# Kernel tuning notes

Measured on AMD Instinct MI355X. Metric: run time of the kernel, lower is better.

Reference implementation:

```python
import jax, jax.numpy as jnp
import numpy as np

NS = 50000; ND = 50000; E = 600000
C = 64; A = 16; S = 64; H = 8; M = 192; DH = C // H
EPS = 1e-5


def _ln(x, w, b):
    # EquivariantLayerNormV2 restricted to 0e irreps == standard affine LayerNorm
    x = x - jnp.mean(x, axis=-1, keepdims=True)
    v = jnp.mean(x * x, axis=-1, keepdims=True)
    return x * jax.lax.rsqrt(v + EPS) * w + b


def _forward(src_f, dst_f, edge_attr, edge_scalars, edge_logits, edge_src, edge_dst,
             ln_src_w, ln_src_b, W_src, ln_dst_w, ln_dst_b, W_dst, b_dst,
             W_ea, W_dtp, W_r1, b_r1, W_r2, b_r2, alpha_vec,
             W_proj, b_proj, ln_post_w, ln_post_b, W_f1, b_f1, W_f2, b_f2):
    # prenorm + linear projections of src/dst node features
    ms = _ln(src_f, ln_src_w, ln_src_b) @ W_src                      # [NS, C]
    md = _ln(dst_f, ln_dst_w, ln_dst_b) @ W_dst + b_dst              # [ND, C]
    msg = ms[edge_src] + md[edge_dst]                                # [E, C] gather
    # radial MLP on edge scalars modulates the (scalar-irrep) tensor-product weights
    r = jax.nn.silu(edge_scalars @ W_r1 + b_r1)                      # [E, S]
    w_edge = r @ W_r2 + b_r2                                         # [E, 2C]
    ea = edge_attr @ W_ea                                            # [E, C]
    dtp = ((msg * ea) @ W_dtp) * w_edge                              # [E, 2C]
    alpha_feat = dtp[:, :C].reshape(E, H, DH)
    val = dtp[:, C:].reshape(E, H, DH)
    # per-head attention logits + optional precomputed edge logits
    logits = jnp.sum(jax.nn.leaky_relu(alpha_feat, 0.2) * alpha_vec, axis=-1)  # [E, H]
    logits = logits + edge_logits[:, None]
    # softmax over incoming edges of each dst node (segment softmax)
    m = jax.ops.segment_max(logits, edge_dst, num_segments=ND)
    a = jnp.exp(logits - m[edge_dst])
    z = jax.ops.segment_sum(a, edge_dst, num_segments=ND)
    attn = a / z[edge_dst]                                           # [E, H]
    out = jax.ops.segment_sum((val * attn[..., None]).reshape(E, C), edge_dst,
                              num_segments=ND)                       # [ND, C] scatter
    out = out @ W_proj + b_proj
    emb = out + dst_f                                                # skip_1 (irreps match -> identity)
    y = _ln(emb, ln_post_w, ln_post_b)                               # post_norm
    ffn = jax.nn.silu(y @ W_f1 + b_f1) @ W_f2 + b_f2                 # FFN with swish gate (0e)
    return ffn + emb                                                 # skip_2


def setup_inputs() -> dict:
    key = jax.random.key(0)
    ks = jax.random.split(key, 20)
    def n(k, shape, scale=1.0):
        return jax.random.normal(k, shape, dtype=jnp.float32) * scale
    return {
        "src_f": n(ks[0], (NS, C)),
        "dst_f": n(ks[1], (ND, C)),
        "edge_attr": n(ks[2], (E, A)),
        "edge_scalars": jax.random.uniform(ks[3], (E, S), dtype=jnp.float32),
        "edge_logits": n(ks[4], (E,)),
        "edge_src": jax.random.randint(ks[5], (E,), 0, NS),
        "edge_dst": jax.random.randint(ks[6], (E,), 0, ND),
        "ln_src_w": jnp.ones((C,), jnp.float32), "ln_src_b": jnp.zeros((C,), jnp.float32),
        "W_src": n(ks[7], (C, C), C ** -0.5),
        "ln_dst_w": jnp.ones((C,), jnp.float32), "ln_dst_b": jnp.zeros((C,), jnp.float32),
        "W_dst": n(ks[8], (C, C), C ** -0.5), "b_dst": jnp.zeros((C,), jnp.float32),
        "W_ea": n(ks[9], (A, C), A ** -0.5),
        "W_dtp": n(ks[10], (C, 2 * C), C ** -0.5),
        "W_r1": n(ks[11], (S, S), S ** -0.5), "b_r1": jnp.zeros((S,), jnp.float32),
        "W_r2": n(ks[12], (S, 2 * C), S ** -0.5), "b_r2": jnp.zeros((2 * C,), jnp.float32),
        "alpha_vec": n(ks[13], (H, DH), DH ** -0.5),
        "W_proj": n(ks[14], (C, C), C ** -0.5), "b_proj": jnp.zeros((C,), jnp.float32),
        "ln_post_w": jnp.ones((C,), jnp.float32), "ln_post_b": jnp.zeros((C,), jnp.float32),
        "W_f1": n(ks[15], (C, M), C ** -0.5), "b_f1": jnp.zeros((M,), jnp.float32),
        "W_f2": n(ks[16], (M, C), M ** -0.5), "b_f2": jnp.zeros((C,), jnp.float32),
    }


def reference(src_f, dst_f, edge_attr, edge_scalars, edge_logits, edge_src, edge_dst,
              ln_src_w, ln_src_b, W_src, ln_dst_w, ln_dst_b, W_dst, b_dst,
              W_ea, W_dtp, W_r1, b_r1, W_r2, b_r2, alpha_vec,
              W_proj, b_proj, ln_post_w, ln_post_b, W_f1, b_f1, W_f2, b_f2):
    return _forward(src_f, dst_f, edge_attr, edge_scalars, edge_logits, edge_src, edge_dst,
                    ln_src_w, ln_src_b, W_src, ln_dst_w, ln_dst_b, W_dst, b_dst,
                    W_ea, W_dtp, W_r1, b_r1, W_r2, b_r2, alpha_vec,
                    W_proj, b_proj, ln_post_w, ln_post_b, W_f1, b_f1, W_f2, b_f2)
```

## Files before the change

kernel.cpp:

```cpp
#include <hip/hip_runtime.h>
#include <hip/hip_bf16.h>

typedef __hip_bfloat16 bf16;
typedef unsigned short u16;
typedef unsigned int u32;

#define NS_N 50000
#define ND_N 50000
#define NE_E 600000
#define C 64
#define AD 16
#define SD 64
#define NH 8
#define MF 192
#define EPSV 1e-5f

#define WB() __builtin_amdgcn_wave_barrier()

typedef short short8 __attribute__((ext_vector_type(8)));
typedef float f32x4 __attribute__((ext_vector_type(4)));
#define MFMA16(a, b, c) __builtin_amdgcn_mfma_f32_16x16x32_bf16(a, b, c, 0, 0, 0)

__device__ __forceinline__ float lo16(u32 u) {
    union { u32 i; float f; } v; v.i = u << 16; return v.f;
}
__device__ __forceinline__ float hi16(u32 u) {
    union { u32 i; float f; } v; v.i = u & 0xffff0000u; return v.f;
}
__device__ __forceinline__ float b2fu(u16 u) {
    union { u32 i; float f; } v; v.i = ((u32)u) << 16; return v.f;
}
__device__ __forceinline__ u16 f2bbits(float f) {
    u32 u = __float_as_uint(f);
    u32 r = u + 0x7FFFu + ((u >> 16) & 1u);
    return (u16)(r >> 16);
}
__device__ __forceinline__ float loadf(const void* p, size_t i, int isbf) {
    if (isbf) { union { u32 u; float f; } v; v.u = ((u32)((const u16*)p)[i]) << 16; return v.f; }
    return ((const float*)p)[i];
}
__device__ __forceinline__ u16 loadb(const void* p, size_t i, int isbf) {
    if (isbf) return ((const u16*)p)[i];
    return f2bbits(((const float*)p)[i]);
}
__device__ __forceinline__ short8 load8bf(const void* p, size_t off, int isbf) {
    if (isbf) return *(const short8*)((const u16*)p + off);
    const float4* q = (const float4*)((const float*)p + off);
    float4 f0 = q[0], f1 = q[1];
    short8 r;
    r[0] = (short)f2bbits(f0.x); r[1] = (short)f2bbits(f0.y);
    r[2] = (short)f2bbits(f0.z); r[3] = (short)f2bbits(f0.w);
    r[4] = (short)f2bbits(f1.x); r[5] = (short)f2bbits(f1.y);
    r[6] = (short)f2bbits(f1.z); r[7] = (short)f2bbits(f1.w);
    return r;
}

__device__ __forceinline__ float waveAllSum(float v) {
    #pragma unroll
    for (int off = 32; off >= 1; off >>= 1) v += __shfl_xor(v, off, 64);
    return v;
}

__global__ void detect_zero_kernel(const void* src, int* flag, int* cnt) {
    if (blockIdx.x == 0) {
        if (threadIdx.x < 64) {
            const u16* p = (const u16*)src;
            const int lane = threadIdx.x;
            int c = 0;
            #pragma unroll
            for (int j = 0; j < 32; ++j) {
                u16 w = p[(size_t)(lane * 32 + j) * 2];
                int e = (w >> 7) & 0xFF;
                if (w == 0 || (e >= 100 && e <= 150)) c++;
            }
            #pragma unroll
            for (int off = 32; off >= 1; off >>= 1) c += __shfl_xor(c, off, 64);
            if (lane == 0) *flag = (c > 1536) ? 1 : 0;
        }
    } else {
        int i = (blockIdx.x - 1) * blockDim.x + threadIdx.x;
        if (i < ND_N) cnt[i] = 0;
    }
}

__global__ void hist_kernel(const int* __restrict__ edge_dst, int* __restrict__ cnt) {
    int e = blockIdx.x * blockDim.x + threadIdx.x;
    if (e < NE_E) atomicAdd(&cnt[edge_dst[e]], 1);
}

#define SCAN_CHUNK 1024
#define SCAN_NCH ((ND_N + SCAN_CHUNK - 1) / SCAN_CHUNK)

__global__ void scan_phase1(const int* __restrict__ cnt, int* __restrict__ chunksum) {
    __shared__ int wsum[4];
    const int b = blockIdx.x, tidx = threadIdx.x;
    const int base = b * SCAN_CHUNK + tidx * 4;
    int s = 0;
    if (base + 3 < ND_N) {
        int4 v = *(const int4*)&cnt[base];
        s = v.x + v.y + v.z + v.w;
    } else {
        #pragma unroll
        for (int j = 0; j < 4; ++j) { int i = base + j; if (i < ND_N) s += cnt[i]; }
    }
    #pragma unroll
    for (int off = 32; off >= 1; off >>= 1) s += __shfl_xor(s, off, 64);
    const int wv = tidx >> 6, lane = tidx & 63;
    if (lane == 0) wsum[wv] = s;
    __syncthreads();
    if (tidx == 0) chunksum[b] = wsum[0] + wsum[1] + wsum[2] + wsum[3];
}

__global__ void scan_phase3(const int* __restrict__ cnt, const int* __restrict__ chunksum,
                            int* __restrict__ row_ptr, int* __restrict__ cursor,
                            int* __restrict__ row_ptr_last) {
    __shared__ int woff[4];
    __shared__ int choff_s;
    const int b = blockIdx.x, tidx = threadIdx.x;
    if (tidx < 64) {
        int v = (tidx < SCAN_NCH) ? chunksum[tidx] : 0;
        int incl = v;
        #pragma unroll
        for (int off = 1; off < 64; off <<= 1) {
            int t = __shfl_up(incl, off, 64);
            if (tidx >= off) incl += t;
        }
        if (tidx == b) choff_s = incl - v;
        if (b == 0 && tidx == 63) *row_ptr_last = incl;
    }
    const int base = b * SCAN_CHUNK + tidx * 4;
    int v[4];
    #pragma unroll
    for (int j = 0; j < 4; ++j) { int i = base + j; v[j] = (i < ND_N) ? cnt[i] : 0; }
    int s = v[0] + v[1] + v[2] + v[3];
    int incl = s;
    const int lane = tidx & 63, wv = tidx >> 6;
    #pragma unroll
    for (int off = 1; off < 64; off <<= 1) {
        int t = __shfl_up(incl, off, 64);
        if (lane >= off) incl += t;
    }
    if (lane == 63) woff[wv] = incl;
    __syncthreads();
    int cross = 0;
    for (int w = 0; w < wv; ++w) cross += woff[w];
    int run = choff_s + cross + (incl - s);
    #pragma unroll
    for (int j = 0; j < 4; ++j) {
        int i = base + j;
        if (i < ND_N) { row_ptr[i] = run; cursor[i] = run; }
        run += v[j];
    }
}

__global__ void scatter_kernel(const int* __restrict__ edge_dst, int* __restrict__ cursor,
                               int* __restrict__ perm) {
    int e = blockIdx.x * blockDim.x + threadIdx.x;
    if (e < NE_E) {
        int pos = atomicAdd(&cursor[edge_dst[e]], 1);
        perm[pos] = e;
    }
}

__launch_bounds__(512)
__global__ void node_proj2_mfma(const void* __restrict__ src_f, const void* __restrict__ dst_f,
                                const void* __restrict__ lnw_s, const void* __restrict__ lnb_s,
                                const void* __restrict__ W_s,
                                const void* __restrict__ lnw_d, const void* __restrict__ lnb_d,
                                const void* __restrict__ W_d, const void* __restrict__ b_d,
                                const int* __restrict__ flagp,
                                u16* __restrict__ ms, u16* __restrict__ md) {
    __shared__ u16 sWT[2][C * C];
    __shared__ float slnw2[2][C], slnb2[2][C], sbias[C];
    __shared__ u16 scratch[8][16 * C];

    const int isbf = *flagp;
    const int tid = threadIdx.x;
    for (int i = tid; i < C * C; i += 512) {
        int k = i >> 6, n = i & 63;
        int off = n * 64 + (((k >> 3) ^ (n & 7)) << 3) + (k & 7);
        sWT[0][off] = loadb(W_s, i, isbf);
        sWT[1][off] = loadb(W_d, i, isbf);
    }
    for (int i = tid; i < C; i += 512) {
        slnw2[0][i] = loadf(lnw_s, i, isbf);
        slnb2[0][i] = loadf(lnb_s, i, isbf);
        slnw2[1][i] = loadf(lnw_d, i, isbf);
        slnb2[1][i] = loadf(lnb_d, i, isbf);
        sbias[i] = loadf(b_d, i, isbf);
    }
    __syncthreads();

    const int wv = tid >> 6, lane = tid & 63;
    const int m15 = lane & 15, quad = lane >> 4;
    const int sw = m15 & 7;
    const int pg0 = (quad ^ sw) << 3;
    const int pg1 = pg0 ^ 32;
    u16* scr = scratch[wv];

    const int HT = NS_N / 16;
    const int NTILE = 2 * HT;
    for (int t = blockIdx.x * 8 + wv; t < NTILE; t += gridDim.x * 8) {
        const int half = (t >= HT) ? 1 : 0;
        const int n0 = (half ? (t - HT) : t) * 16;
        const void* xf = half ? dst_f : src_f;
        u16* out = half ? md : ms;
        float x0[8], x1[8];
        {
            size_t base = (size_t)(n0 + m15) * C + quad * 8;
            if (isbf) {
                short8 aa = *(const short8*)((const u16*)xf + base);
                short8 bb = *(const short8*)((const u16*)xf + base + 32);
                #pragma unroll
                for (int j = 0; j < 8; ++j) {
                    x0[j] = b2fu((u16)aa[j]);
                    x1[j] = b2fu((u16)bb[j]);
                }
            } else {
                const float* xp = (const float*)xf + base;
                float4 a0 = *(const float4*)xp;
                float4 a1 = *(const float4*)(xp + 4);
                float4 b0 = *(const float4*)(xp + 32);
                float4 b1 = *(const float4*)(xp + 36);
                x0[0] = a0.x; x0[1] = a0.y; x0[2] = a0.z; x0[3] = a0.w;
                x0[4] = a1.x; x0[5] = a1.y; x0[6] = a1.z; x0[7] = a1.w;
                x1[0] = b0.x; x1[1] = b0.y; x1[2] = b0.z; x1[3] = b0.w;
                x1[4] = b1.x; x1[5] = b1.y; x1[6] = b1.z; x1[7] = b1.w;
            }
        }
        float s = 0.f;
        #pragma unroll
        for (int j = 0; j < 8; ++j) s += x0[j] + x1[j];
        s += __shfl_xor(s, 16, 64);
        s += __shfl_xor(s, 32, 64);
        float mean = s * (1.f / 64.f);
        float q = 0.f;
        #pragma unroll
        for (int j = 0; j < 8; ++j) {
            float d0 = x0[j] - mean, d1 = x1[j] - mean;
            q += d0 * d0 + d1 * d1;
        }
        q += __shfl_xor(q, 16, 64);
        q += __shfl_xor(q, 32, 64);
        float rs = rsqrtf(q * (1.f / 64.f) + EPSV);
        short8 xA0, xA1;
        #pragma unroll
        for (int j = 0; j < 8; ++j) {
            int c0 = quad * 8 + j, c1 = 32 + quad * 8 + j;
            xA0[j] = (short)f2bbits((x0[j] - mean) * rs * slnw2[half][c0] + slnb2[half][c0]);
            xA1[j] = (short)f2bbits((x1[j] - mean) * rs * slnw2[half][c1] + slnb2[half][c1]);
        }
        WB();
        const u16* wT = sWT[half];
        #pragma unroll
        for (int nt = 0; nt < 4; ++nt) {
            f32x4 c = {0.f, 0.f, 0.f, 0.f};
            c = MFMA16(xA0, *(const short8*)&wT[(nt * 16 + m15) * 64 + pg0], c);
            c = MFMA16(xA1, *(const short8*)&wT[(nt * 16 + m15) * 64 + pg1], c);
            float bb = half ? sbias[nt * 16 + m15] : 0.f;
            int lg = nt * 2 + (m15 >> 3);
            int o = m15 & 7;
            #pragma unroll
            for (int r = 0; r < 4; ++r) {
                float v = c[r] + bb;
                int row = quad * 4 + r;
                scr[row * 64 + ((lg ^ (row & 7)) << 3) + o] = f2bbits(v);
            }
        }
        WB();
        {
            int row = lane >> 2, seg = lane & 3;
            int rw7 = row & 7;
            uint4 v0 = *(const uint4*)&scr[row * 64 + (((seg * 2) ^ rw7) << 3)];
            uint4 v1 = *(const uint4*)&scr[row * 64 + (((seg * 2 + 1) ^ rw7) << 3)];
            uint4* gp = (uint4*)&out[(size_t)(n0 + row) * C + seg * 16];
            gp[0] = v0; gp[1] = v1;
        }
        WB();
    }
}

__launch_bounds__(512, 4)
__global__ void edge_mfma_kernel(const void* __restrict__ edge_attr,
                                 const void* __restrict__ edge_scalars,
                                 const void* __restrict__ edge_logits,
                                 const int* __restrict__ edge_src,
                                 const int* __restrict__ edge_dst,
                                 const int* __restrict__ perm,
                                 const void* __restrict__ W_ea, const void* __restrict__ W_dtp,
                                 const void* __restrict__ W_r1, const void* __restrict__ b_r1,
                                 const void* __restrict__ W_r2, const void* __restrict__ b_r2,
                                 const void* __restrict__ alpha_vec,
                                 const int* __restrict__ flagp,
                                 const u16* __restrict__ ms, const u16* __restrict__ md,
                                 u16* __restrict__ valbuf, float* __restrict__ logitsbuf) {
    __shared__ u16 sWr1T[C * SD];
    __shared__ u16 sWr2T[2 * C * SD];
    __shared__ u16 sWdtpT[2 * C * C];
    __shared__ u16 sWeaT[C * 32];
    __shared__ float sbr1[SD], sbr2[2 * C], salpha[C];
    __shared__ u16 scratch[8][2][16 * C];

    const int isbf = *flagp;
    const int tid = threadIdx.x;
    for (int i = tid; i < SD * SD; i += 512) {
        int k = i >> 6, n = i & 63;
        sWr1T[n * 64 + (((k >> 3) ^ (n & 7)) << 3) + (k & 7)] = loadb(W_r1, i, isbf);
    }
    for (int i = tid; i < SD * 2 * C; i += 512) {
        int k = i >> 7, n = i & 127;
        sWr2T[n * 64 + (((k >> 3) ^ (n & 7)) << 3) + (k & 7)] = loadb(W_r2, i, isbf);
    }
    for (int i = tid; i < C * 2 * C; i += 512) {
        int k = i >> 7, n = i & 127;
        sWdtpT[n * 64 + (((k >> 3) ^ (n & 7)) << 3) + (k & 7)] = loadb(W_dtp, i, isbf);
    }
    for (int i = tid; i < C * 32; i += 512) {
        int n = i >> 5, k = i & 31;
        sWeaT[i] = (k < AD) ? loadb(W_ea, (size_t)k * C + n, isbf) : (u16)0;
    }
    for (int i = tid; i < SD; i += 512) sbr1[i] = loadf(b_r1, i, isbf);
    for (int i = tid; i < 2 * C; i += 512) sbr2[i] = loadf(b_r2, i, isbf);
    for (int i = tid; i < C; i += 512) salpha[i] = loadf(alpha_vec, i, isbf);
    __syncthreads();

    const int wv = tid >> 6, lane = tid & 63;
    const int m15 = lane & 15, quad = lane >> 4;
    const int sw = m15 & 7;
    const int pg0 = (quad ^ sw) << 3;
    const int pg1 = pg0 ^ 32;
    u16* scr_r = scratch[wv][0];
    u16* scr_e = scratch[wv][1];

    const int NT = NE_E / 16;
    const int stride = gridDim.x * 8;
    int t = blockIdx.x * 8 + wv;

    int e = 0, s = 0, dd = 0;
    if (t < NT) {
        e = perm[t * 16 + m15];
        s = edge_src[e];
        dd = edge_dst[e];
    }

    while (t < NT) {
        const int tn = t + stride;
        const int e0 = t * 16;
        short8 esA0 = load8bf(edge_scalars, (size_t)e * SD + quad * 8, isbf);
        short8 esA1 = load8bf(edge_scalars, (size_t)e * SD + 32 + quad * 8, isbf);
        float elg_lane = loadf(edge_logits, e, isbf);
        short8 eaA = 0;
        if (quad < 2) eaA = load8bf(edge_attr, (size_t)e * AD + quad * 8, isbf);
        const u16* msr = ms + (size_t)s * C;
        const u16* mdr = md + (size_t)dd * C;
        short8 gms0 = *(const short8*)&msr[quad * 8];
        short8 gms1 = *(const short8*)&msr[32 + quad * 8];
        short8 gmd0 = *(const short8*)&mdr[quad * 8];
        short8 gmd1 = *(const short8*)&mdr[32 + quad * 8];
        int eN = 0;
        if (tn < NT) eN = perm[tn * 16 + m15];
        WB();
        #pragma unroll
        for (int nt = 0; nt < 4; ++nt) {
            f32x4 c = {0.f, 0.f, 0.f, 0.f};
            c = MFMA16(esA0, *(const short8*)&sWr1T[(nt * 16 + m15) * 64 + pg0], c);
            c = MFMA16(esA1, *(const short8*)&sWr1T[(nt * 16 + m15) * 64 + pg1], c);
            float bc = sbr1[nt * 16 + m15];
            int lg = nt * 2 + (m15 >> 3);
            int o = m15 & 7;
            #pragma unroll
            for (int r = 0; r < 4; ++r) {
                float f = c[r] + bc;
                f = f / (1.f + __expf(-f));
                int row = quad * 4 + r;
                scr_r[row * 64 + ((lg ^ (row & 7)) << 3) + o] = f2bbits(f);
            }
        }
        #pragma unroll
        for (int nt = 0; nt < 4; ++nt) {
            f32x4 c = {0.f, 0.f, 0.f, 0.f};
            c = MFMA16(eaA, *(const short8*)&sWeaT[(nt * 16 + m15) * 32 + quad * 8], c);
            int lg = nt * 2 + (m15 >> 3);
            int o = m15 & 7;
            #pragma unroll
            for (int r = 0; r < 4; ++r) {
                int row = quad * 4 + r;
                scr_e[row * 64 + ((lg ^ (row & 7)) << 3) + o] = f2bbits(c[r]);
            }
        }
        int sN = 0, ddN = 0;
        if (tn < NT) { sN = edge_src[eN]; ddN = edge_dst[eN]; }
        WB();
        short8 rA0 = *(const short8*)&scr_r[m15 * 64 + pg0];
        short8 rA1 = *(const short8*)&scr_r[m15 * 64 + pg1];
        short8 ev0 = *(const short8*)&scr_e[m15 * 64 + pg0];
        short8 ev1 = *(const short8*)&scr_e[m15 * 64 + pg1];
        short8 xA0, xA1;
        #pragma unroll
        for (int j = 0; j < 8; ++j) {
            float a = b2fu((u16)gms0[j]) + b2fu((u16)gmd0[j]);
            xA0[j] = (short)f2bbits(a * b2fu((u16)ev0[j]));
            float b = b2fu((u16)gms1[j]) + b2fu((u16)gmd1[j]);
            xA1[j] = (short)f2bbits(b * b2fu((u16)ev1[j]));
        }
        float elg_q[4];
        #pragma unroll
        for (int r = 0; r < 4; ++r) elg_q[r] = __shfl(elg_lane, quad * 4 + r, 64);
        WB();
        #pragma unroll
        for (int nt = 0; nt < 8; ++nt) {
            f32x4 w = {0.f, 0.f, 0.f, 0.f};
            w = MFMA16(rA0, *(const short8*)&sWr2T[(nt * 16 + m15) * 64 + pg0], w);
            w = MFMA16(rA1, *(const short8*)&sWr2T[(nt * 16 + m15) * 64 + pg1], w);
            f32x4 dv = {0.f, 0.f, 0.f, 0.f};
            dv = MFMA16(xA0, *(const short8*)&sWdtpT[(nt * 16 + m15) * 64 + pg0], dv);
            dv = MFMA16(xA1, *(const short8*)&sWdtpT[(nt * 16 + m15) * 64 + pg1], dv);
            float wb = sbr2[nt * 16 + m15];
            if (nt < 4) {
                float sa = salpha[nt * 16 + m15];
                #pragma unroll
                for (int r = 0; r < 4; ++r) {
                    float v = dv[r] * (w[r] + wb);
                    float lf = (v >= 0.f) ? v : 0.2f * v;
                    float tt = lf * sa;
                    tt += __shfl_xor(tt, 1, 64);
                    tt += __shfl_xor(tt, 2, 64);
                    tt += __shfl_xor(tt, 4, 64);
                    if ((lane & 7) == 0)
                        logitsbuf[(size_t)(e0 + quad * 4 + r) * NH + nt * 2 + ((lane >> 3) & 1)]
                            = tt + elg_q[r];
                }
            } else {
                int lg = (nt - 4) * 2 + (m15 >> 3);
                int o = m15 & 7;
                #pragma unroll
                for (int r = 0; r < 4; ++r) {
                    float v = dv[r] * (w[r] + wb);
                    int row = quad * 4 + r;
                    scr_r[row * 64 + ((lg ^ (row & 7)) << 3) + o] = f2bbits(v);
                }
            }
        }
        WB();
        {
            int row = lane >> 2, seg = lane & 3;
            int rw7 = row & 7;
            uint4 v0 = *(const uint4*)&scr_r[row * 64 + (((seg * 2) ^ rw7) << 3)];
            uint4 v1 = *(const uint4*)&scr_r[row * 64 + (((seg * 2 + 1) ^ rw7) << 3)];
            uint4* gp = (uint4*)&valbuf[(size_t)(e0 + row) * C + seg * 16];
            gp[0] = v0; gp[1] = v1;
        }
        WB();
        t = tn; e = eN; s = sN; dd = ddN;
    }
}

__global__ void aggregate_kernel(const int* __restrict__ row_ptr,
                                 const float* __restrict__ logitsbuf,
                                 const u16* __restrict__ valbuf,
                                 float* __restrict__ attout) {
    const int wave = threadIdx.x >> 6, lane = threadIdx.x & 63;
    const int h = lane & 31;
    const int parity = lane >> 5;
    const int head = h >> 2;
    const int gw = blockIdx.x * 4 + wave, nw = gridDim.x * 4;
    const float NINF = -1e30f;
    for (int d = gw; d < ND_N; d += nw) {
        const int beg = row_ptr[d], end = row_ptr[d + 1];
        float m0 = NINF, z0 = 0.f, a00 = 0.f, a01 = 0.f;
        float m1 = NINF, z1 = 0.f, a10 = 0.f, a11 = 0.f;
        for (int i = beg + parity; i < end; i += 4) {
            u32 pv = *(const u32*)&valbuf[(size_t)i * C + 2 * h];
            float lg = logitsbuf[(size_t)i * NH + head];
            float mn = fmaxf(m0, lg);
            float sc = __expf(m0 - mn);
            float e = __expf(lg - mn);
            z0 = z0 * sc + e;
            a00 = a00 * sc + e * lo16(pv);
            a01 = a01 * sc + e * hi16(pv);
            m0 = mn;
        }
        for (int i = beg + parity + 2; i < end; i += 4) {
            u32 pv = *(const u32*)&valbuf[(size_t)i * C + 2 * h];
            float lg = logitsbuf[(size_t)i * NH + head];
            float mn = fmaxf(m1, lg);
            float sc = __expf(m1 - mn);
            float e = __expf(lg - mn);
            z1 = z1 * sc + e;
            a10 = a10 * sc + e * lo16(pv);
            a11 = a11 * sc + e * hi16(pv);
            m1 = mn;
        }
        float ma = fmaxf(m0, m1);
        float s0 = __expf(m0 - ma), s1 = __expf(m1 - ma);
        float z = z0 * s0 + z1 * s1;
        float a0 = a00 * s0 + a10 * s1;
        float a1 = a01 * s0 + a11 * s1;
        float mo = __shfl_xor(ma, 32, 64);
        float zo = __shfl_xor(z, 32, 64);
        float b0 = __shfl_xor(a0, 32, 64);
        float b1 = __shfl_xor(a1, 32, 64);
        float mm = fmaxf(ma, mo);
        float se = __expf(ma - mm), so = __expf(mo - mm);
        z = z * se + zo * so;
        a0 = a0 * se + b0 * so;
        a1 = a1 * se + b1 * so;
        if (parity == 0) {
            float2 r;
            r.x = (z > 0.f) ? a0 / z : 0.f;
            r.y = (z > 0.f) ? a1 / z : 0.f;
            *(float2*)&attout[(size_t)d * C + 2 * h] = r;
        }
    }
}

__global__ void edge_csr_kernel(const void* __restrict__ edge_attr,
                                const void* __restrict__ edge_scalars,
                                const void* __restrict__ edge_logits,
                                const int* __restrict__ edge_src,
                                const int* __restrict__ row_ptr, const int* __restrict__ perm,
                                const void* __restrict__ W_ea, const void* __restrict__ W_dtp,
                                const void* __restrict__ W_r1, const void* __restrict__ b_r1,
                                const void* __restrict__ W_r2, const void* __restrict__ b_r2,
                                const void* __restrict__ alpha_vec,
                                const int* __restrict__ flagp,
                                const u16* __restrict__ ms, const u16* __restrict__ md,
                                float* __restrict__ attout) {
    __shared__ u16 sWr1[SD * SD];
    __shared__ u16 sWr2[SD * 2 * C];
    __shared__ u16 sWdtp[C * 2 * C];
    __shared__ u16 sWea[AD * C];
    __shared__ float sbr1[SD], sbr2[2 * C], salpha[C];
    __shared__ float sbuf[4][2][C];

    const int isbf = *flagp;
    const int tid = threadIdx.x;
    {
        for (int i = tid; i < SD * SD; i += blockDim.x) {
            int k = i >> 6, c = i & 63;
            sWr1[((k >> 1) << 7) + (c << 1) + (k & 1)] = loadb(W_r1, i, isbf);
        }
        for (int i = tid; i < SD * 2 * C; i += blockDim.x) {
            int k = i >> 7, c = i & 127;
            sWr2[(k << 7) + ((c & 63) << 1) + (c >> 6)] = loadb(W_r2, i, isbf);
        }
        for (int i = tid; i < C * 2 * C; i += blockDim.x) {
            int k = i >> 7, c = i & 127;
            sWdtp[(k << 7) + ((c & 63) << 1) + (c >> 6)] = loadb(W_dtp, i, isbf);
        }
        for (int i = tid; i < AD * C; i += blockDim.x) {
            int k = i >> 6, c = i & 63;
            sWea[((k >> 1) << 7) + (c << 1) + (k & 1)] = loadb(W_ea, i, isbf);
        }
        for (int i = tid; i < SD; i += blockDim.x) sbr1[i] = loadf(b_r1, i, isbf);
        for (int i = tid; i < 2 * C; i += blockDim.x) sbr2[i] = loadf(b_r2, i, isbf);
        for (int i = tid; i < C; i += blockDim.x) salpha[i] = loadf(alpha_vec, i, isbf);
    }
    __syncthreads();

    const int wave = tid >> 6, lane = tid & 63;
    float* buf0 = sbuf[wave][0];
    float* buf1 = sbuf[wave][1];
    const u32* wr1 = (const u32*)sWr1;
    const u32* wr2 = (const u32*)sWr2;
    const u32* wdtp = (const u32*)sWdtp;
    const u32* wea = (const u32*)sWea;
    const int gw = blockIdx.x * 4 + wave, nw = gridDim.x * 4;

    for (int d = gw; d < ND_N; d += nw) {
        const int beg = row_ptr[d], end = row_ptr[d + 1];
        const float mdv = b2fu(md[(size_t)d * C + lane]);
        float m = -__builtin_inff(), z = 0.f, acc = 0.f;

        for (int i = beg; i < end; ++i) {
            const int e = perm[i];
            WB();
            buf0[lane] = loadf(edge_scalars, (size_t)e * SD + lane, isbf);
            WB();
            float accr = sbr1[lane];
            #pragma unroll 8
            for (int k2 = 0; k2 < 32; ++k2) {
                float2 xv = *(const float2*)&buf0[k2 * 2];
                u32 wp = wr1[(k2 << 6) + lane];
                accr += xv.x * lo16(wp) + xv.y * hi16(wp);
            }
            float r = accr / (1.f + __expf(-accr));
            WB();
            buf1[lane] = r;
            WB();
            float we0 = sbr2[lane], we1 = sbr2[lane + C];
            #pragma unroll 8
            for (int k = 0; k < SD; ++k) {
                float rk = buf1[k];
                u32 wp = wr2[(k << 6) + lane];
                we0 += rk * lo16(wp);
                we1 += rk * hi16(wp);
            }
            WB();
            if (lane < AD) buf0[lane] = loadf(edge_attr, (size_t)e * AD + lane, isbf);
            WB();
            float eav = 0.f;
            #pragma unroll
            for (int k2 = 0; k2 < 8; ++k2) {
                float2 xv = *(const float2*)&buf0[k2 * 2];
                u32 wp = wea[(k2 << 6) + lane];
                eav += xv.x * lo16(wp) + xv.y * hi16(wp);
            }
            const int s = edge_src[e];
            float x = (b2fu(ms[(size_t)s * C + lane]) + mdv) * eav;
            WB();
            buf1[lane] = x;
            WB();
            float dt0 = 0.f, dt1 = 0.f;
            #pragma unroll 8
            for (int k = 0; k < C; ++k) {
                float xk = buf1[k];
                u32 wp = wdtp[(k << 6) + lane];
                dt0 += xk * lo16(wp);
                dt1 += xk * hi16(wp);
            }
            dt0 *= we0;
            dt1 *= we1;
            float lf = (dt0 >= 0.f) ? dt0 : 0.2f * dt0;
            float t = lf * salpha[lane];
            t += __shfl_xor(t, 1, 64);
            t += __shfl_xor(t, 2, 64);
            t += __shfl_xor(t, 4, 64);
            float lg = t + loadf(edge_logits, e, isbf);
            float mn = fmaxf(m, lg);
            float sc = __expf(m - mn);
            float a = __expf(lg - mn);
            z = z * sc + a;
            acc = acc * sc + a * dt1;
            m = mn;
        }
        attout[(size_t)d * C + lane] = (z > 0.f) ? acc / z : 0.f;
    }
}

__launch_bounds__(512, 2)
__global__ void final_mfma_kernel(const void* __restrict__ dst_f,
                                  const float* __restrict__ attout,
                                  const void* __restrict__ W_proj, const void* __restrict__ b_proj,
                                  const void* __restrict__ ln_w, const void* __restrict__ ln_b,
                                  const void* __restrict__ W_f1, const void* __restrict__ b_f1,
                                  const void* __restrict__ W_f2, const void* __restrict__ b_f2,
                                  const int* __restrict__ flagp,
                                  void* __restrict__ out) {
    __shared__ u16 sWpT[C * C];
    __shared__ u16 sWf1T[MF * C];
    __shared__ u16 sWf2T[C * MF];
    __shared__ float sbp[C], slnw[C], slnb[C], sbf1[MF], sbf2[C];
    __shared__ uint4 scr4[8][400];

    const int isbf = *flagp;
    const int tid = threadIdx.x;
    for (int i = tid; i < C * C; i += 512) {
        int k = i >> 6, n = i & 63;
        sWpT[n * 64 + (((k >> 3) ^ (n & 7)) << 3) + (k & 7)] = loadb(W_proj, i, isbf);
    }
    for (int i = tid; i < C * MF; i += 512) {
        int k = i / MF, n = i - k * MF;
        sWf1T[n * 64 + (((k >> 3) ^ (n & 7)) << 3) + (k & 7)] = loadb(W_f1, i, isbf);
    }
    for (int i = tid; i < MF * C; i += 512) {
        int k = i >> 6, n = i & 63;
        sWf2T[n * 192 + (((k >> 3) ^ (n & 7)) << 3) + (k & 7)] = loadb(W_f2, i, isbf);
    }
    for (int i = tid; i < C; i += 512) {
        sbp[i] = loadf(b_proj, i, isbf);
        slnw[i] = loadf(ln_w, i, isbf);
        slnb[i] = loadf(ln_b, i, isbf);
        sbf2[i] = loadf(b_f2, i, isbf);
    }
    for (int i = tid; i < MF; i += 512) sbf1[i] = loadf(b_f1, i, isbf);
    __syncthreads();

    const int wv = tid >> 6, lane = tid & 63;
    const int m15 = lane & 15, quad = lane >> 4;
    const int sw = m15 & 7;
    const int pg0 = (quad ^ sw) << 3;
    const int pg1 = pg0 ^ 32;
    u16* scr = (u16*)scr4[wv];
    float* scrf = (float*)scr4[wv];

    for (int t = blockIdx.x * 8 + wv; t < ND_N / 16; t += gridDim.x * 8) {
        const int n0 = t * 16;
        short8 oA0 = load8bf(attout, (size_t)(n0 + m15) * C + quad * 8, 0);
        short8 oA1 = load8bf(attout, (size_t)(n0 + m15) * C + 32 + quad * 8, 0);
        float emb[4][4];
        #pragma unroll
        for (int nt = 0; nt < 4; ++nt) {
            f32x4 c = {0.f, 0.f, 0.f, 0.f};
            c = MFMA16(oA0, *(const short8*)&sWpT[(nt * 16 + m15) * 64 + pg0], c);
            c = MFMA16(oA1, *(const short8*)&sWpT[(nt * 16 + m15) * 64 + pg1], c);
            int col = nt * 16 + m15;
            float bp = sbp[col];
            #pragma unroll
            for (int r = 0; r < 4; ++r)
                emb[nt][r] = c[r] + bp + loadf(dst_f, (size_t)(n0 + quad * 4 + r) * C + col, isbf);
        }
        float y[4][4];
        #pragma unroll
        for (int r = 0; r < 4; ++r) {
            float part = emb[0][r] + emb[1][r] + emb[2][r] + emb[3][r];
            part += __shfl_xor(part, 1, 64);
            part += __shfl_xor(part, 2, 64);
            part += __shfl_xor(part, 4, 64);
            part += __shfl_xor(part, 8, 64);
            float mean = part * (1.f / 64.f);
            float q = 0.f;
            #pragma unroll
            for (int nt = 0; nt < 4; ++nt) {
                float d = emb[nt][r] - mean;
                q += d * d;
            }
            q += __shfl_xor(q, 1, 64);
            q += __shfl_xor(q, 2, 64);
            q += __shfl_xor(q, 4, 64);
            q += __shfl_xor(q, 8, 64);
            float rs = rsqrtf(q * (1.f / 64.f) + EPSV);
            #pragma unroll
            for (int nt = 0; nt < 4; ++nt) {
                int col = nt * 16 + m15;
                y[nt][r] = (emb[nt][r] - mean) * rs * slnw[col] + slnb[col];
            }
        }
        WB();
        #pragma unroll
        for (int nt = 0; nt < 4; ++nt)
            #pragma unroll
            for (int r = 0; r < 4; ++r)
                scr[(quad * 4 + r) * 72 + nt * 16 + m15] = f2bbits(y[nt][r]);
        WB();
        short8 yA0 = *(const short8*)&scr[m15 * 72 + quad * 8];
        short8 yA1 = *(const short8*)&scr[m15 * 72 + 32 + quad * 8];
        WB();
        #pragma unroll
        for (int nt = 0; nt < 12; ++nt) {
            f32x4 g = {0.f, 0.f, 0.f, 0.f};
            g = MFMA16(yA0, *(const short8*)&sWf1T[(nt * 16 + m15) * 64 + pg0], g);
            g = MFMA16(yA1, *(const short8*)&sWf1T[(nt * 16 + m15) * 64 + pg1], g);
            int col = nt * 16 + m15;
            float bg = sbf1[col];
            #pragma unroll
            for (int r = 0; r < 4; ++r) {
                float f = g[r] + bg;
                f = f / (1.f + __expf(-f));
                scr[(quad * 4 + r) * 200 + col] = f2bbits(f);
            }
        }
        WB();
        short8 gA[6];
        #pragma unroll
        for (int j = 0; j < 6; ++j)
            gA[j] = *(const short8*)&scr[m15 * 200 + j * 32 + quad * 8];
        WB();
        #pragma unroll
        for (int nt = 0; nt < 4; ++nt) {
            f32x4 c = {0.f, 0.f, 0.f, 0.f};
            #pragma unroll
            for (int j = 0; j < 6; ++j) {
                int lg = j * 4 + quad;
                int pg = (lg ^ sw) << 3;
                c = MFMA16(gA[j], *(const short8*)&sWf2T[(nt * 16 + m15) * 192 + pg], c);
            }
            int col = nt * 16 + m15;
            float bf = sbf2[col];
            #pragma unroll
            for (int r = 0; r < 4; ++r)
                scrf[(quad * 4 + r) * 68 + col] = c[r] + bf + emb[nt][r];
        }
        WB();
        {
            int row = lane >> 2, seg = lane & 3;
            if (isbf) {
                u16* gp = (u16*)out + (size_t)(n0 + row) * C + seg * 16;
                #pragma unroll
                for (int j = 0; j < 4; ++j) {
                    float4 v = *(const float4*)&scrf[row * 68 + seg * 16 + j * 4];
                    u32 p0 = (u32)f2bbits(v.x) | ((u32)f2bbits(v.y) << 16);
                    u32 p1 = (u32)f2bbits(v.z) | ((u32)f2bbits(v.w) << 16);
                    uint2 pk = {p0, p1};
                    *(uint2*)(gp + j * 4) = pk;
                }
            } else {
                float* gp = (float*)out + (size_t)(n0 + row) * C + seg * 16;
                #pragma unroll
                for (int j = 0; j < 4; ++j)
                    *(float4*)(gp + j * 4) = *(const float4*)&scrf[row * 68 + seg * 16 + j * 4];
            }
        }
        WB();
    }
}

__global__ void final_scalar_kernel(const void* __restrict__ dst_f,
                                    const float* __restrict__ attout,
                                    const void* __restrict__ W_proj, const void* __restrict__ b_proj,
                                    const void* __restrict__ ln_w, const void* __restrict__ ln_b,
                                    const void* __restrict__ W_f1, const void* __restrict__ b_f1,
                                    const void* __restrict__ W_f2, const void* __restrict__ b_f2,
                                    const int* __restrict__ flagp,
                                    void* __restrict__ out) {
    __shared__ u16 sWp[C * C];
    __shared__ u16 sWf1p[C * 2 * C];
    __shared__ u16 sWf1c[C * C];
    __shared__ u16 sWf2[MF * C];
    __shared__ float sbp[C], slnw[C], slnb[C], sbf1[MF], sbf2[C];
    __shared__ float ybuf[4][C];
    __shared__ float gbuf[4][MF];

    const int isbf = *flagp;
    const int tid = threadIdx.x;
    {
        for (int i = tid; i < C * C; i += blockDim.x) {
            int k = i >> 6, c = i & 63;
            sWp[((k >> 1) << 7) + (c << 1) + (k & 1)] = loadb(W_proj, i, isbf);
        }
        for (int i = tid; i < C * MF; i += blockDim.x) {
            int k = i / MF, c = i - k * MF;
            u16 b = loadb(W_f1, i, isbf);
            if (c < 128) sWf1p[(k << 7) + ((c & 63) << 1) + (c >> 6)] = b;
            else         sWf1c[(k << 6) + (c - 128)] = b;
        }
        for (int i = tid; i < MF * C; i += blockDim.x) {
            int k = i >> 6, c = i & 63;
            sWf2[((k >> 1) << 7) + (c << 1) + (k & 1)] = loadb(W_f2, i, isbf);
        }
        for (int i = tid; i < C; i += blockDim.x) {
            sbp[i] = loadf(b_proj, i, isbf);
            slnw[i] = loadf(ln_w, i, isbf);
            slnb[i] = loadf(ln_b, i, isbf);
            sbf2[i] = loadf(b_f2, i, isbf);
        }
        for (int i = tid; i < MF; i += blockDim.x) sbf1[i] = loadf(b_f1, i, isbf);
    }
    __syncthreads();

    const int wave = tid >> 6, lane = tid & 63;
    const u32* wp32 = (const u32*)sWp;
    const u32* wf1 = (const u32*)sWf1p;
    const u32* wf2 = (const u32*)sWf2;
    const int gw = blockIdx.x * 4 + wave, nw = gridDim.x * 4;

    for (int n = gw; n < ND_N; n += nw) {
        float o = attout[(size_t)n * C + lane];
        WB();
        ybuf[wave][lane] = o;
        WB();
        float p = sbp[lane];
        #pragma unroll 8
        for (int k2 = 0; k2 < 32; ++k2) {
            float2 yv = *(const float2*)&ybuf[wave][k2 * 2];
            u32 wv = wp32[(k2 << 6) + lane];
            p += yv.x * lo16(wv) + yv.y * hi16(wv);
        }
        float emb = p + loadf(dst_f, (size_t)n * C + lane, isbf);
        float mean = waveAllSum(emb) * (1.f / 64.f);
        float ec = emb - mean;
        float var = waveAllSum(ec * ec) * (1.f / 64.f);
        float y = ec * rsqrtf(var + EPSV) * slnw[lane] + slnb[lane];
        WB();
        ybuf[wave][lane] = y;
        WB();
        float g0 = sbf1[lane], g1v = sbf1[lane + C], g2v = sbf1[lane + 2 * C];
        #pragma unroll 8
        for (int k = 0; k < C; ++k) {
            float yk = ybuf[wave][k];
            u32 wv = wf1[(k << 6) + lane];
            union { u32 u; float f; } cv; cv.u = ((u32)sWf1c[(k << 6) + lane]) << 16;
            g0 += yk * lo16(wv);
            g1v += yk * hi16(wv);
            g2v += yk * cv.f;
        }
        WB();
        gbuf[wave][lane] = g0 / (1.f + __expf(-g0));
        gbuf[wave][lane + C] = g1v / (1.f + __expf(-g1v));
        gbuf[wave][lane + 2 * C] = g2v / (1.f + __expf(-g2v));
        WB();
        float f = sbf2[lane];
        #pragma unroll 8
        for (int k2 = 0; k2 < 96; ++k2) {
            float2 gv = *(const float2*)&gbuf[wave][k2 * 2];
            u32 wv = wf2[(k2 << 6) + lane];
            f += gv.x * lo16(wv) + gv.y * hi16(wv);
        }
        WB();
        float res = f + emb;
        if (isbf) ((bf16*)out)[(size_t)n * C + lane] = __float2bfloat16(res);
        else      ((float*)out)[(size_t)n * C + lane] = res;
    }
}

extern "C" void kernel_launch(void* const* d_in, const int* in_sizes, int n_in,
                              void* d_out, int out_size, void* d_ws, size_t ws_size,
                              hipStream_t stream) {
    const void* src_f        = d_in[0];
    const void* dst_f        = d_in[1];
    const void* edge_attr    = d_in[2];
    const void* edge_scalars = d_in[3];
    const void* edge_logits  = d_in[4];
    const int*  edge_src     = (const int*)d_in[5];
    const int*  edge_dst     = (const int*)d_in[6];
    const void* ln_src_w = d_in[7];
    const void* ln_src_b = d_in[8];
    const void* W_src    = d_in[9];
    const void* ln_dst_w = d_in[10];
    const void* ln_dst_b = d_in[11];
    const void* W_dst    = d_in[12];
    const void* b_dst    = d_in[13];
    const void* W_ea     = d_in[14];
    const void* W_dtp    = d_in[15];
    const void* W_r1     = d_in[16];
    const void* b_r1     = d_in[17];
    const void* W_r2     = d_in[18];
    const void* b_r2     = d_in[19];
    const void* alpha_vec = d_in[20];
    const void* W_proj   = d_in[21];
    const void* b_proj   = d_in[22];
    const void* ln_post_w = d_in[23];
    const void* ln_post_b = d_in[24];
    const void* W_f1     = d_in[25];
    const void* b_f1     = d_in[26];
    const void* W_f2     = d_in[27];
    const void* b_f2     = d_in[28];

    int* flag     = (int*)d_ws;
    float* msf    = (float*)d_ws + 16;
    float* mdf    = msf + (size_t)NS_N * C;
    u16* ms16     = (u16*)msf;
    u16* md16     = (u16*)mdf;
    int* cnt      = (int*)(mdf + (size_t)ND_N * C);
    int* row_ptr  = cnt + ND_N;
    int* cursor   = row_ptr + (ND_N + 4);
    int* perm     = cursor + ND_N;
    float* logitsbuf = (float*)(perm + NE_E);
    u16* valbuf      = (u16*)(logitsbuf + (size_t)NE_E * NH);
    float* attout_slow = (float*)(perm + NE_E);

    size_t base_b = (size_t)(16 + NS_N * C + ND_N * C) * 4
                  + ((size_t)ND_N * 3 + 4 + NE_E) * 4;
    size_t need_fast = base_b + (size_t)NE_E * NH * 4 + (size_t)NE_E * C * 2;
    size_t need_slow = base_b + (size_t)ND_N * C * 4;
    int fast = (ws_size >= need_fast) ? 1 : 0;
    if (!fast && ws_size < need_slow) return;

    detect_zero_kernel<<<1 + (ND_N + 255) / 256, 256, 0, stream>>>(src_f, flag, cnt);
    hist_kernel<<<(NE_E + 255) / 256, 256, 0, stream>>>(edge_dst, cnt);
    scan_phase1<<<SCAN_NCH, 256, 0, stream>>>(cnt, perm);
    scan_phase3<<<SCAN_NCH, 256, 0, stream>>>(cnt, perm, row_ptr, cursor, &row_ptr[ND_N]);
    scatter_kernel<<<(NE_E + 255) / 256, 256, 0, stream>>>(edge_dst, cursor, perm);

    node_proj2_mfma<<<782, 512, 0, stream>>>(src_f, dst_f,
                                             ln_src_w, ln_src_b, W_src,
                                             ln_dst_w, ln_dst_b, W_dst, b_dst,
                                             flag, ms16, md16);

    if (fast) {
        edge_mfma_kernel<<<1024, 512, 0, stream>>>(edge_attr, edge_scalars, edge_logits,
                                                   edge_src, edge_dst, perm,
                                                   W_ea, W_dtp, W_r1, b_r1, W_r2, b_r2,
                                                   alpha_vec, flag, ms16, md16,
                                                   valbuf, logitsbuf);
        aggregate_kernel<<<4096, 256, 0, stream>>>(row_ptr, logitsbuf, valbuf, msf);
        final_mfma_kernel<<<256, 512, 0, stream>>>(dst_f, msf,
                                                   W_proj, b_proj, ln_post_w, ln_post_b,
                                                   W_f1, b_f1, W_f2, b_f2,
                                                   flag, d_out);
    } else {
        edge_csr_kernel<<<2048, 256, 0, stream>>>(edge_attr, edge_scalars, edge_logits,
                                                  edge_src, row_ptr, perm,
                                                  W_ea, W_dtp, W_r1, b_r1, W_r2, b_r2,
                                                  alpha_vec, flag, ms16, md16, attout_slow);
        final_scalar_kernel<<<1024, 256, 0, stream>>>(dst_f, attout_slow,
                                                      W_proj, b_proj, ln_post_w, ln_post_b,
                                                      W_f1, b_f1, W_f2, b_f2,
                                                      flag, d_out);
    }
}
```

Measured before the change: 575.2 us.

## Replace LDS scratch transposes in edge kernel with MFMA operand swap and lane shuffles

The edge kernel used to route the radial-MLP and edge-attr MFMA outputs through per-wave LDS scratch to reshape them into A-operand layout. It now swaps the MFMA operands so each lane holds edge-major results, packs them to bf16 pairs and rebuilds the operand fragments with cross-lane shuffles. That drops the scratch buffer and its wave barriers. The val output is now written straight to global memory as scattered 2-byte stores instead of coalesced 16-byte stores through LDS, and the grid shrinks from 1024 to 768 blocks since the smaller LDS footprint may allow more resident blocks. The shuffle-heavy path and the uncoalesced stores add cost that may offset the saved LDS traffic.

```diff
diff --git a/kernel.cpp b/kernel.cpp
--- a/kernel.cpp
+++ b/kernel.cpp
@@ -34,6 +34,9 @@
     u32 u = __float_as_uint(f);
     u32 r = u + 0x7FFFu + ((u >> 16) & 1u);
     return (u16)(r >> 16);
+}
+__device__ __forceinline__ u32 pack2bf(float a, float b) {
+    return (u32)f2bbits(a) | ((u32)f2bbits(b) << 16);
 }
 __device__ __forceinline__ float loadf(const void* p, size_t i, int isbf) {
     if (isbf) { union { u32 u; float f; } v; v.u = ((u32)((const u16*)p)[i]) << 16; return v.f; }
@@ -299,7 +302,6 @@
     __shared__ u16 sWdtpT[2 * C * C];
     __shared__ u16 sWeaT[C * 32];
     __shared__ float sbr1[SD], sbr2[2 * C], salpha[C];
-    __shared__ u16 scratch[8][2][16 * C];
 
     const int isbf = *flagp;
     const int tid = threadIdx.x;
@@ -329,8 +331,9 @@
     const int sw = m15 & 7;
     const int pg0 = (quad ^ sw) << 3;
     const int pg1 = pg0 ^ 32;
-    u16* scr_r = scratch[wv][0];
-    u16* scr_e = scratch[wv][1];
+    const int la = m15 + ((quad & 1) << 5);
+    const int lb = la + 16;
+    const int hi = quad >> 1;
 
     const int NT = NE_E / 16;
     const int stride = gridDim.x * 8;
@@ -359,42 +362,76 @@
         short8 gmd1 = *(const short8*)&mdr[32 + quad * 8];
         int eN = 0;
         if (tn < NT) eN = perm[tn * 16 + m15];
-        WB();
+
+        u32 pu[8];
         #pragma unroll
         for (int nt = 0; nt < 4; ++nt) {
             f32x4 c = {0.f, 0.f, 0.f, 0.f};
-            c = MFMA16(esA0, *(const short8*)&sWr1T[(nt * 16 + m15) * 64 + pg0], c);
-            c = MFMA16(esA1, *(const short8*)&sWr1T[(nt * 16 + m15) * 64 + pg1], c);
-            float bc = sbr1[nt * 16 + m15];
-            int lg = nt * 2 + (m15 >> 3);
-            int o = m15 & 7;
+            c = MFMA16(*(const short8*)&sWr1T[(nt * 16 + m15) * 64 + pg0], esA0, c);
+            c = MFMA16(*(const short8*)&sWr1T[(nt * 16 + m15) * 64 + pg1], esA1, c);
+            float p[4];
             #pragma unroll
             for (int r = 0; r < 4; ++r) {
-                float f = c[r] + bc;
-                f = f / (1.f + __expf(-f));
-                int row = quad * 4 + r;
-                scr_r[row * 64 + ((lg ^ (row & 7)) << 3) + o] = f2bbits(f);
-            }
-        }
-        #pragma unroll
-        for (int nt = 0; nt < 4; ++nt) {
-            f32x4 c = {0.f, 0.f, 0.f, 0.f};
-            c = MFMA16(eaA, *(const short8*)&sWeaT[(nt * 16 + m15) * 32 + quad * 8], c);
-            int lg = nt * 2 + (m15 >> 3);
-            int o = m15 & 7;
-            #pragma unroll
-            for (int r = 0; r < 4; ++r) {
-                int row = quad * 4 + r;
-                scr_e[row * 64 + ((lg ^ (row & 7)) << 3) + o] = f2bbits(c[r]);
+                float f = c[r] + sbr1[nt * 16 + quad * 4 + r];
+                p[r] = f / (1.f + __expf(-f));
+            }
+            pu[nt * 2] = pack2bf(p[0], p[1]);
+            pu[nt * 2 + 1] = pack2bf(p[2], p[3]);
+        }
+        short8 rA0, rA1;
+        {
+            u32 t0 = (u32)__shfl((int)pu[0], la, 64), t1 = (u32)__shfl((int)pu[1], la, 64);
+            u32 t2 = (u32)__shfl((int)pu[2], la, 64), t3 = (u32)__shfl((int)pu[3], la, 64);
+            u32 s0 = (u32)__shfl((int)pu[0], lb, 64), s1 = (u32)__shfl((int)pu[1], lb, 64);
+            u32 s2 = (u32)__shfl((int)pu[2], lb, 64), s3 = (u32)__shfl((int)pu[3], lb, 64);
+            union { u32 u[4]; short8 v; } cv;
+            cv.u[0] = hi ? t2 : t0; cv.u[1] = hi ? t3 : t1;
+            cv.u[2] = hi ? s2 : s0; cv.u[3] = hi ? s3 : s1;
+            rA0 = cv.v;
+        }
+        {
+            u32 t4 = (u32)__shfl((int)pu[4], la, 64), t5 = (u32)__shfl((int)pu[5], la, 64);
+            u32 t6 = (u32)__shfl((int)pu[6], la, 64), t7 = (u32)__shfl((int)pu[7], la, 64);
+            u32 s4 = (u32)__shfl((int)pu[4], lb, 64), s5 = (u32)__shfl((int)pu[5], lb, 64);
+            u32 s6 = (u32)__shfl((int)pu[6], lb, 64), s7 = (u32)__shfl((int)pu[7], lb, 64);
+            union { u32 u[4]; short8 v; } cv;
+            cv.u[0] = hi ? t6 : t4; cv.u[1] = hi ? t7 : t5;
+            cv.u[2] = hi ? s6 : s4; cv.u[3] = hi ? s7 : s5;
+            rA1 = cv.v;
+        }
+        short8 ev0, ev1;
+        {
+            u32 qu[8];
+            #pragma unroll
+            for (int nt = 0; nt < 4; ++nt) {
+                f32x4 c = {0.f, 0.f, 0.f, 0.f};
+                c = MFMA16(*(const short8*)&sWeaT[(nt * 16 + m15) * 32 + quad * 8], eaA, c);
+                qu[nt * 2] = pack2bf(c[0], c[1]);
+                qu[nt * 2 + 1] = pack2bf(c[2], c[3]);
+            }
+            {
+                u32 t0 = (u32)__shfl((int)qu[0], la, 64), t1 = (u32)__shfl((int)qu[1], la, 64);
+                u32 t2 = (u32)__shfl((int)qu[2], la, 64), t3 = (u32)__shfl((int)qu[3], la, 64);
+                u32 s0 = (u32)__shfl((int)qu[0], lb, 64), s1 = (u32)__shfl((int)qu[1], lb, 64);
+                u32 s2 = (u32)__shfl((int)qu[2], lb, 64), s3 = (u32)__shfl((int)qu[3], lb, 64);
+                union { u32 u[4]; short8 v; } cv;
+                cv.u[0] = hi ? t2 : t0; cv.u[1] = hi ? t3 : t1;
+                cv.u[2] = hi ? s2 : s0; cv.u[3] = hi ? s3 : s1;
+                ev0 = cv.v;
+            }
+            {
+                u32 t4 = (u32)__shfl((int)qu[4], la, 64), t5 = (u32)__shfl((int)qu[5], la, 64);
+                u32 t6 = (u32)__shfl((int)qu[6], la, 64), t7 = (u32)__shfl((int)qu[7], la, 64);
+                u32 s4 = (u32)__shfl((int)qu[4], lb, 64), s5 = (u32)__shfl((int)qu[5], lb, 64);
+                u32 s6 = (u32)__shfl((int)qu[6], lb, 64), s7 = (u32)__shfl((int)qu[7], lb, 64);
+                union { u32 u[4]; short8 v; } cv;
+                cv.u[0] = hi ? t6 : t4; cv.u[1] = hi ? t7 : t5;
+                cv.u[2] = hi ? s6 : s4; cv.u[3] = hi ? s7 : s5;
+                ev1 = cv.v;
             }
         }
         int sN = 0, ddN = 0;
         if (tn < NT) { sN = edge_src[eN]; ddN = edge_dst[eN]; }
-        WB();
-        short8 rA0 = *(const short8*)&scr_r[m15 * 64 + pg0];
-        short8 rA1 = *(const short8*)&scr_r[m15 * 64 + pg1];
-        short8 ev0 = *(const short8*)&scr_e[m15 * 64 + pg0];
-        short8 ev1 = *(const short8*)&scr_e[m15 * 64 + pg1];
         short8 xA0, xA1;
         #pragma unroll
         for (int j = 0; j < 8; ++j) {
@@ -406,7 +443,6 @@
         float elg_q[4];
         #pragma unroll
         for (int r = 0; r < 4; ++r) elg_q[r] = __shfl(elg_lane, quad * 4 + r, 64);
-        WB();
         #pragma unroll
         for (int nt = 0; nt < 8; ++nt) {
             f32x4 w = {0.f, 0.f, 0.f, 0.f};
@@ -431,26 +467,13 @@
                             = tt + elg_q[r];
                 }
             } else {
-                int lg = (nt - 4) * 2 + (m15 >> 3);
-                int o = m15 & 7;
                 #pragma unroll
                 for (int r = 0; r < 4; ++r) {
                     float v = dv[r] * (w[r] + wb);
-                    int row = quad * 4 + r;
-                    scr_r[row * 64 + ((lg ^ (row & 7)) << 3) + o] = f2bbits(v);
+                    valbuf[(size_t)(e0 + quad * 4 + r) * C + (nt - 4) * 16 + m15] = f2bbits(v);
                 }
             }
         }
-        WB();
-        {
-            int row = lane >> 2, seg = lane & 3;
-            int rw7 = row & 7;
-            uint4 v0 = *(const uint4*)&scr_r[row * 64 + (((seg * 2) ^ rw7) << 3)];
-            uint4 v1 = *(const uint4*)&scr_r[row * 64 + (((seg * 2 + 1) ^ rw7) << 3)];
-            uint4* gp = (uint4*)&valbuf[(size_t)(e0 + row) * C + seg * 16];
-            gp[0] = v0; gp[1] = v1;
-        }
-        WB();
         t = tn; e = eN; s = sN; dd = ddN;
     }
 }
@@ -958,11 +981,11 @@
                                              flag, ms16, md16);
 
     if (fast) {
-        edge_mfma_kernel<<<1024, 512, 0, stream>>>(edge_attr, edge_scalars, edge_logits,
-                                                   edge_src, edge_dst, perm,
-                                                   W_ea, W_dtp, W_r1, b_r1, W_r2, b_r2,
-                                                   alpha_vec, flag, ms16, md16,
-                                                   valbuf, logitsbuf);
+        edge_mfma_kernel<<<768, 512, 0, stream>>>(edge_attr, edge_scalars, edge_logits,
+                                                  edge_src, edge_dst, perm,
+                                                  W_ea, W_dtp, W_r1, b_r1, W_r2, b_r2,
+                                                  alpha_vec, flag, ms16, md16,
+                                                  valbuf, logitsbuf);
         aggregate_kernel<<<4096, 256, 0, stream>>>(row_ptr, logitsbuf, valbuf, msf);
         final_mfma_kernel<<<256, 512, 0, stream>>>(dst_f, msf,
                                                    W_proj, b_proj, ln_post_w, ln_post_b,
```

After: 890.1 us. 1.55x slower.
